# Kernel optimization log

Measured on AMD Instinct MI355X. Metric: run time of the kernel, lower is better.

## Reference

```python
import jax, jax.numpy as jnp
import numpy as np

N_NODES, N_EDGES, NNZ = 10000, 4000, 30000
IN_CH, HEADS, OUT_CH = 128, 2, 64


def _scale2_pattern(node, edge, num_nodes, num_edges):
    """Sparsity pattern of H @ (H^T H) where H is the node x edge incidence.
    Mirrors torch.sparse.mm + coalesce + (values > 0) mask (pattern only,
    since all values are positive sums of ones)."""
    # unique incidence pattern (coalesce)
    uk = np.unique(node.astype(np.int64) * num_edges + edge.astype(np.int64))
    n_u, e_u = uk // num_edges, uk % num_edges
    # --- stage 1: pattern of H^T H = edge pairs sharing a node ---
    order = np.argsort(n_u, kind="stable")
    ns, es = n_u[order], e_u[order]
    _, starts, cnts = np.unique(ns, return_index=True, return_counts=True)
    cpe = np.repeat(cnts, cnts)          # group size per sorted entry
    gpe = np.repeat(starts, cnts)        # group start per sorted entry
    tot = int(cpe.sum())
    within = np.arange(tot) - np.repeat(np.cumsum(cpe) - cpe, cpe)
    pe = np.repeat(es, cpe)
    pep = es[np.repeat(gpe, cpe) + within]
    pk = np.unique(pe * num_edges + pep)
    pe, pep = pk // num_edges, pk % num_edges
    # --- stage 2: pattern of H @ (H^T H) ---
    po = np.argsort(pe, kind="stable")
    pe_s, pep_s = pe[po], pep[po]
    cnt_e = np.bincount(pe_s, minlength=num_edges)
    ptr = np.concatenate([np.zeros(1, np.int64), np.cumsum(cnt_e)])
    c2 = cnt_e[e_u]
    tot2 = int(c2.sum())
    within2 = np.arange(tot2) - np.repeat(np.cumsum(c2) - c2, c2)
    v2 = np.repeat(n_u, c2)
    ep2 = pep_s[ptr[e_u].repeat(c2) + within2]
    k2 = np.unique(v2 * num_edges + ep2)
    return k2 // num_edges, k2 % num_edges


def setup_inputs() -> dict:
    rng = np.random.default_rng(0)
    node1 = rng.integers(0, N_NODES, NNZ).astype(np.int64)
    edge1 = rng.integers(0, N_EDGES, NNZ).astype(np.int64)
    node2, edge2 = _scale2_pattern(node1, edge1, N_NODES, N_EDGES)

    key = jax.random.key(0)
    k = jax.random.split(key, 4)
    HO = HEADS * OUT_CH
    xav1 = (2.0 / (IN_CH + HO)) ** 0.5
    xavo = (2.0 / (HO + OUT_CH)) ** 0.5
    return {
        "x": jax.random.normal(k[0], (N_NODES, IN_CH), jnp.float32),
        "hyperedge_index1": jnp.asarray(np.stack([node1, edge1]), jnp.int32),
        "hyperedge_index2": jnp.asarray(np.stack([node2, edge2]), jnp.int32),
        "W1": jax.random.normal(k[1], (HO, IN_CH), jnp.float32) * xav1,
        "b1": jnp.zeros((HO,), jnp.float32),
        "W2": jax.random.normal(k[2], (HO, IN_CH), jnp.float32) * xav1,
        "b2": jnp.zeros((HO,), jnp.float32),
        "Wout": jax.random.normal(k[3], (OUT_CH, HO), jnp.float32) * xavo,
        "bout": jnp.zeros((OUT_CH,), jnp.float32),
        "num_edges": N_EDGES,
    }


def _hconv(x, W, b, node_idx, edge_idx, num_edges):
    num_nodes = x.shape[0]
    xt = x @ W.T + b                                  # [N, H*O]
    g = xt[node_idx]                                  # [nnz, H*O] gather
    esum = jax.ops.segment_sum(g, edge_idx, num_segments=num_edges)
    cnt = jax.ops.segment_sum(jnp.ones(edge_idx.shape, xt.dtype), edge_idx,
                              num_segments=num_edges)
    emean = esum / jnp.maximum(cnt, 1.0)[:, None]     # scatter_mean (0 if empty)
    return jax.ops.segment_sum(emean[edge_idx], node_idx,
                               num_segments=num_nodes)  # scatter_add


def reference(x, hyperedge_index1, hyperedge_index2, W1, b1, W2, b2, Wout, bout,
              num_edges):
    o1 = _hconv(x, W1, b1, hyperedge_index1[0], hyperedge_index1[1], num_edges)
    o2 = _hconv(x, W2, b2, hyperedge_index2[0], hyperedge_index2[1], num_edges)
    o = 0.5 * (o1 + o2)                               # mean over 2 scales
    return o @ Wout.T + bout                          # output_proj
```

## Files before the change

kernel.cpp:

```cpp
#include <hip/hip_runtime.h>
#include <hip/hip_bf16.h>

#define N_NODES 10000
#define N_EDGES 4000
#define IN_CH   128
#define HOC     128
#define OUT_CH  64
#define CHUNK   16384

#define G_GEMM  625
#define G_NPTR  40

__device__ __forceinline__ float bf2f(unsigned short u) {
    union { unsigned int i; float f; } v;
    v.i = ((unsigned int)u) << 16;
    return v.f;
}
__device__ __forceinline__ unsigned short f2bfu(float f) {
    union { __hip_bfloat16 h; unsigned short u; } v;
    v.h = __float2bfloat16(f);
    return v.u;
}

__device__ __forceinline__ void load8(const void* base, size_t eoff, int isf32,
                                      float o[8]) {
    if (isf32) {
        const float4* q = (const float4*)((const float*)base + eoff);
        float4 a = q[0], b = q[1];
        o[0]=a.x; o[1]=a.y; o[2]=a.z; o[3]=a.w;
        o[4]=b.x; o[5]=b.y; o[6]=b.z; o[7]=b.w;
    } else {
        uint4 v = *(const uint4*)((const unsigned short*)base + eoff);
        const unsigned short* pv = (const unsigned short*)&v;
#pragma unroll
        for (int q = 0; q < 8; q++) o[q] = bf2f(pv[q]);
    }
}

__device__ __forceinline__ float loadS(const void* base, int i, int isf32) {
    return isf32 ? ((const float*)base)[i] : bf2f(((const unsigned short*)base)[i]);
}

__device__ __forceinline__ int probe_isf32(const unsigned int* __restrict__ x) {
    const int lane = threadIdx.x & 63;
    unsigned int w0 = x[lane * 2], w1 = x[lane * 2 + 1];
    int h = 0, z = 0;
    {
        unsigned int lo = w0 & 0xFFFFu;
        if (lo == 0u) z++; else if (((lo >> 7) & 0xFF) >= 0x90u) h++;
        lo = w1 & 0xFFFFu;
        if (lo == 0u) z++; else if (((lo >> 7) & 0xFF) >= 0x90u) h++;
    }
    unsigned long long bh = __ballot(h > 0);
    unsigned long long bz = __ballot(z == 2);
    return (__popcll(bh) > 8 || __popcll(bz) > 50) ? 1 : 0;
}

__device__ __forceinline__ void add4(float acc[4], uint2 u) {
    acc[0] += bf2f((unsigned short)(u.x & 0xFFFFu));
    acc[1] += bf2f((unsigned short)(u.x >> 16));
    acc[2] += bf2f((unsigned short)(u.y & 0xFFFFu));
    acc[3] += bf2f((unsigned short)(u.y >> 16));
}

__global__ __launch_bounds__(256) void weff_zero(
    const void* __restrict__ Wout,
    const void* __restrict__ W1, const void* __restrict__ b1,
    const void* __restrict__ W2, const void* __restrict__ b2,
    float* __restrict__ weff1, float* __restrict__ beff1,
    float* __restrict__ weff2, float* __restrict__ beff2,
    int* __restrict__ cntz, int* __restrict__ fillz,
    const unsigned int* __restrict__ xprobe)
{
    const int b = blockIdx.x;
    if (b == 16) {
        for (int t = threadIdx.x; t < 18000; t += 256) cntz[t] = 0;
        for (int t = threadIdx.x; t < 14000; t += 256) fillz[t] = 0;
        return;
    }
    const int isf32 = probe_isf32(xprobe);
    if (b == 17) {
        const int t = threadIdx.x;
        if (t < 128) {
            const int s = t >> 6, o = t & 63;
            const void* bs = s ? b2 : b1;
            float a = 0.f;
            for (int h = 0; h < 128; h++)
                a += loadS(Wout, o * 128 + h, isf32) * loadS(bs, h, isf32);
            (s ? beff2 : beff1)[o] = 0.5f * a;
        }
        return;
    }
    const int s = b >> 3;
    const void* Ws = s ? W2 : W1;
    float* outW = s ? weff2 : weff1;
    const int o  = (b & 7) * 8 + (threadIdx.x >> 5);
    const int i0 = (threadIdx.x & 31) * 4;
    float acc[4] = {0.f, 0.f, 0.f, 0.f};
    for (int h = 0; h < 128; h++) {
        float wo = loadS(Wout, o * 128 + h, isf32);
        acc[0] += wo * loadS(Ws, h * 128 + i0 + 0, isf32);
        acc[1] += wo * loadS(Ws, h * 128 + i0 + 1, isf32);
        acc[2] += wo * loadS(Ws, h * 128 + i0 + 2, isf32);
        acc[3] += wo * loadS(Ws, h * 128 + i0 + 3, isf32);
    }
    *(float4*)(outW + o * 128 + i0) =
        make_float4(0.5f * acc[0], 0.5f * acc[1], 0.5f * acc[2], 0.5f * acc[3]);
}

__global__ __launch_bounds__(256) void prep(
    const void* __restrict__ x,
    const float* __restrict__ weff1, const float* __restrict__ beff1,
    const float* __restrict__ weff2, const float* __restrict__ beff2,
    unsigned short* __restrict__ xtP1b, unsigned short* __restrict__ xtP2b,
    const int* __restrict__ idx1, int nnz1,
    const int* __restrict__ idx2, int nnz2,
    int* __restrict__ nptr,
    int* __restrict__ bh, int* __restrict__ cnt2,
    int* __restrict__ cnt1e, int* __restrict__ cnt1n, int nblk)
{
    __shared__ __align__(16) char smem[40000];
    int b = blockIdx.x;

    if (b < nblk) {
        int* h = (int*)smem;
        for (int t = threadIdx.x; t < N_EDGES; t += 256) h[t] = 0;
        __syncthreads();
        const int lo = b * CHUNK;
        const int hi = min(nnz2, lo + CHUNK);
        for (int i = lo + threadIdx.x; i < hi; i += 256)
            atomicAdd(&h[idx2[nnz2 + i]], 1);
        __syncthreads();
        int* dst = bh + (size_t)b * N_EDGES;
        for (int t = threadIdx.x; t < N_EDGES; t += 256) {
            int v = h[t];
            dst[t] = v;
            if (v) atomicAdd(&cnt2[t], v);
        }
        return;
    }
    b -= nblk;

    if (b < 8) {
        const int isEdge = b < 4;
        const int bid = isEdge ? b : (b - 4);
        const int nb = isEdge ? N_EDGES : N_NODES;
        const int* src = isEdge ? (idx1 + nnz1) : idx1;
        int* dst = isEdge ? cnt1e : cnt1n;
        int* h = (int*)smem;
        for (int t = threadIdx.x; t < nb; t += 256) h[t] = 0;
        __syncthreads();
        for (int i = bid * 256 + threadIdx.x; i < nnz1; i += 4 * 256)
            atomicAdd(&h[src[i]], 1);
        __syncthreads();
        for (int t = threadIdx.x; t < nb; t += 256) {
            int v = h[t];
            if (v) atomicAdd(&dst[t], v);
        }
        return;
    }
    b -= 8;

    if (b < G_GEMM) {
        const int isf32 = probe_isf32((const unsigned int*)x);
        float (*xs)[IN_CH] = (float (*)[IN_CH])smem;
        const int n0 = b * 16;
        {
            float v[8];
            load8(x, (size_t)n0 * IN_CH + (size_t)threadIdx.x * 8, isf32, v);
            float* dst = &xs[0][0] + threadIdx.x * 8;
#pragma unroll
            for (int q = 0; q < 8; q++) dst[q] = v[q];
        }
        __syncthreads();

        const int g   = threadIdx.x >> 7;
        const int sel = (threadIdx.x >> 6) & 1;
        const int j   = threadIdx.x & 63;
        const float* WE = sel ? weff2 : weff1;
        const float* BE = sel ? beff2 : beff1;
        unsigned short* xtP = sel ? xtP2b : xtP1b;

        float acc[8];
#pragma unroll
        for (int m = 0; m < 8; m++) acc[m] = 0.f;

        const float4* Wr = (const float4*)(WE + (size_t)j * 128);
        for (int kk = 0; kk < 16; kk++) {
            float4 a = Wr[kk * 2], c = Wr[kk * 2 + 1];
            float w[8] = {a.x, a.y, a.z, a.w, c.x, c.y, c.z, c.w};
#pragma unroll
            for (int m = 0; m < 8; m++) {
                const float* xr = &xs[g * 8 + m][kk * 8];
                acc[m] += xr[0]*w[0] + xr[1]*w[1] + xr[2]*w[2] + xr[3]*w[3]
                        + xr[4]*w[4] + xr[5]*w[5] + xr[6]*w[6] + xr[7]*w[7];
            }
        }
        const float bias = BE[j];
#pragma unroll
        for (int m = 0; m < 8; m++)
            xtP[(size_t)(n0 + g * 8 + m) * 64 + j] = f2bfu(acc[m] + bias);
        return;
    }
    b -= G_GEMM;

    {
        int n = b * 256 + threadIdx.x;
        if (n > N_NODES) return;
        int lo = 0, hi = nnz2;
        while (lo < hi) { int mid = (lo + hi) >> 1; if (idx2[mid] < n) lo = mid + 1; else hi = mid; }
        nptr[n] = lo;
    }
}

__global__ __launch_bounds__(256) void scans3(
    const int* __restrict__ cnt2, int* __restrict__ ptr2,
    const int* __restrict__ cnt1e, int* __restrict__ ptr1e,
    const int* __restrict__ cnt1n, int* __restrict__ ptr1n)
{
    const int* cnt; int* ptr; int nb;
    if (blockIdx.x == 0)      { cnt = cnt2;  ptr = ptr2;  nb = N_EDGES; }
    else if (blockIdx.x == 1) { cnt = cnt1e; ptr = ptr1e; nb = N_EDGES; }
    else                      { cnt = cnt1n; ptr = ptr1n; nb = N_NODES; }
    __shared__ int part[256];
    const int t = threadIdx.x;
    const int K = (nb + 255) >> 8;
    const int base = t * K;
    int s = 0;
    for (int q = 0; q < K; q++) {
        int i = base + q;
        s += (i < nb) ? cnt[i] : 0;
    }
    part[t] = s;
    __syncthreads();
    for (int d = 1; d < 256; d <<= 1) {
        int v = (t >= d) ? part[t - d] : 0;
        __syncthreads();
        part[t] += v;
        __syncthreads();
    }
    int run = part[t] - s;
    for (int q = 0; q < K; q++) {
        int i = base + q;
        if (i < nb) { ptr[i] = run; run += cnt[i]; }
    }
    if (t == 255) ptr[nb] = part[255];
}

__global__ __launch_bounds__(256) void sb_fb(
    const int* __restrict__ ptr2, int* __restrict__ bh, int nblk,
    const int* __restrict__ idx1, int nnz1,
    const int* __restrict__ ptr1e, int* __restrict__ fill1e,
    unsigned short* __restrict__ nodelist1,
    const int* __restrict__ ptr1n, int* __restrict__ fill1n,
    unsigned short* __restrict__ edgelist1)
{
    int b = blockIdx.x;
    if (b < 16) {
        int e = b * 256 + threadIdx.x;
        if (e >= N_EDGES) return;
        int run = ptr2[e];
        int k = 0;
        for (; k + 8 <= nblk; k += 8) {
            int v[8];
#pragma unroll
            for (int q = 0; q < 8; q++)
                v[q] = bh[(size_t)(k + q) * N_EDGES + e];
#pragma unroll
            for (int q = 0; q < 8; q++) {
                bh[(size_t)(k + q) * N_EDGES + e] = run;
                run += v[q];
            }
        }
        for (; k < nblk; k++) {
            int i = k * N_EDGES + e;
            int t = bh[i];
            bh[i] = run;
            run += t;
        }
        return;
    }
    b -= 16;
    int i = b * 256 + threadIdx.x;
    if (i >= nnz1) return;
    int n = idx1[i];
    int e = idx1[nnz1 + i];
    int se = atomicAdd(&fill1e[e], 1);
    nodelist1[ptr1e[e] + se] = (unsigned short)n;
    int sn = atomicAdd(&fill1n[n], 1);
    edgelist1[ptr1n[n] + sn] = (unsigned short)e;
}

__global__ __launch_bounds__(1024) void place_entries(
    const int* __restrict__ idx, int nnz, const int* __restrict__ bh,
    unsigned short* __restrict__ nodelist)
{
    __shared__ int lh[N_EDGES];
    for (int t = threadIdx.x; t < N_EDGES; t += 1024) lh[t] = 0;
    __syncthreads();
    const int b = blockIdx.x;
    const int lo = b * CHUNK;
    const int hi = min(nnz, lo + CHUNK);
    const int* bhb = bh + (size_t)b * N_EDGES;
    for (int i = lo + threadIdx.x; i < hi; i += 1024) {
        int n = idx[i];
        int e = idx[nnz + i];
        int s = atomicAdd(&lh[e], 1);
        nodelist[bhb[e] + s] = (unsigned short)n;
    }
}

__global__ __launch_bounds__(256) void edge_gather(
    const unsigned short* __restrict__ nodelist2, const int* __restrict__ ptr2,
    const unsigned int* __restrict__ xtP2u, unsigned int* __restrict__ emean2b,
    const unsigned short* __restrict__ nodelist1, const int* __restrict__ ptr1e,
    const unsigned int* __restrict__ xtP1u, unsigned int* __restrict__ emean1b)
{
    int b = blockIdx.x;
    if (b < 1000) {
        const int lane = threadIdx.x & 63;
        const int sub  = lane >> 4;
        const int ch4  = lane & 15;
        const int e = b * 4 + (threadIdx.x >> 6);
        const int lo = ptr2[e], hi = ptr2[e + 1];
        const uint2* src2 = (const uint2*)xtP2u;
        float acc[4] = {0.f, 0.f, 0.f, 0.f};
        int i = lo;
        for (; i + 32 <= hi; i += 32) {
            int n[8]; uint2 u[8];
#pragma unroll
            for (int q = 0; q < 8; q++) n[q] = nodelist2[i + 4 * q + sub];
#pragma unroll
            for (int q = 0; q < 8; q++) u[q] = src2[(size_t)n[q] * 16 + ch4];
#pragma unroll
            for (int q = 0; q < 8; q++) add4(acc, u[q]);
        }
        for (; i < hi; i += 4) {
            if (i + sub < hi) {
                int n0 = nodelist2[i + sub];
                add4(acc, src2[(size_t)n0 * 16 + ch4]);
            }
        }
#pragma unroll
        for (int q = 0; q < 4; q++) {
            acc[q] += __shfl_xor(acc[q], 16);
            acc[q] += __shfl_xor(acc[q], 32);
        }
        if (sub == 0) {
            const float inv = 1.f / fmaxf((float)(hi - lo), 1.f);
            uint2 o;
            o.x = ((unsigned int)f2bfu(acc[1] * inv) << 16) | f2bfu(acc[0] * inv);
            o.y = ((unsigned int)f2bfu(acc[3] * inv) << 16) | f2bfu(acc[2] * inv);
            ((uint2*)emean2b)[(size_t)e * 16 + ch4] = o;
        }
        return;
    }
    b -= 1000;
    {
        const int lane = threadIdx.x & 31;
        const int e = b * 8 + (threadIdx.x >> 5);
        const int lo = ptr1e[e], hi = ptr1e[e + 1];
        float accx = 0.f, accy = 0.f;
        for (int base = lo; base < hi; base += 32) {
            const int m = min(32, hi - base);
            int vl = (base + lane < hi) ? (int)nodelist1[base + lane] : 0;
            int t = 0;
            for (; t + 7 < m; t += 8) {
                int nn[8]; unsigned int uu[8];
#pragma unroll
                for (int q = 0; q < 8; q++) nn[q] = __shfl(vl, t + q, 32);
#pragma unroll
                for (int q = 0; q < 8; q++) uu[q] = xtP1u[nn[q] * 32 + lane];
#pragma unroll
                for (int q = 0; q < 8; q++) {
                    accx += bf2f((unsigned short)(uu[q] & 0xFFFFu));
                    accy += bf2f((unsigned short)(uu[q] >> 16));
                }
            }
            for (; t < m; t++) {
                int n = __shfl(vl, t, 32);
                unsigned int u = xtP1u[n * 32 + lane];
                accx += bf2f((unsigned short)(u & 0xFFFFu));
                accy += bf2f((unsigned short)(u >> 16));
            }
        }
        const float inv = 1.f / fmaxf((float)(hi - lo), 1.f);
        emean1b[e * 32 + lane] =
            ((unsigned int)f2bfu(accy * inv) << 16) | f2bfu(accx * inv);
    }
}

__global__ __launch_bounds__(256) void node_final(
    const int* __restrict__ vals2, const int* __restrict__ nptr,
    const unsigned int* __restrict__ emean2b,
    const unsigned short* __restrict__ edgelist1, const int* __restrict__ ptr1n,
    const unsigned int* __restrict__ emean1b,
    const void* __restrict__ bout, void* __restrict__ out,
    const unsigned int* __restrict__ xprobe)
{
    const int isf32 = probe_isf32(xprobe);
    const int lane = threadIdx.x & 63;
    const int sub  = lane >> 4;
    const int ch4  = lane & 15;
    const int n = blockIdx.x * 4 + (threadIdx.x >> 6);
    float acc[4] = {0.f, 0.f, 0.f, 0.f};

    {
        const int lo = nptr[n], hi = nptr[n + 1];
        const uint2* src = (const uint2*)emean2b;
        int i = lo;
        for (; i + 32 <= hi; i += 32) {
            int e[8]; uint2 u[8];
#pragma unroll
            for (int q = 0; q < 8; q++) e[q] = vals2[i + 4 * q + sub];
#pragma unroll
            for (int q = 0; q < 8; q++) u[q] = src[(size_t)e[q] * 16 + ch4];
#pragma unroll
            for (int q = 0; q < 8; q++) add4(acc, u[q]);
        }
        for (; i < hi; i += 4) {
            if (i + sub < hi)
                add4(acc, src[(size_t)vals2[i + sub] * 16 + ch4]);
        }
    }
    {
        const int lo = ptr1n[n], hi = ptr1n[n + 1];
        const uint2* src = (const uint2*)emean1b;
        int i = lo;
        for (; i + 32 <= hi; i += 32) {
            int e[8]; uint2 u[8];
#pragma unroll
            for (int q = 0; q < 8; q++) e[q] = edgelist1[i + 4 * q + sub];
#pragma unroll
            for (int q = 0; q < 8; q++) u[q] = src[(size_t)e[q] * 16 + ch4];
#pragma unroll
            for (int q = 0; q < 8; q++) add4(acc, u[q]);
        }
        for (; i < hi; i += 4) {
            if (i + sub < hi)
                add4(acc, src[(size_t)edgelist1[i + sub] * 16 + ch4]);
        }
    }
#pragma unroll
    for (int q = 0; q < 4; q++) {
        acc[q] += __shfl_xor(acc[q], 16);
        acc[q] += __shfl_xor(acc[q], 32);
    }
    if (sub == 0) {
        float r[4];
#pragma unroll
        for (int q = 0; q < 4; q++)
            r[q] = acc[q] + loadS(bout, ch4 * 4 + q, isf32);
        if (isf32) {
            ((float4*)out)[(size_t)n * 16 + ch4] =
                make_float4(r[0], r[1], r[2], r[3]);
        } else {
            uint2 o;
            o.x = ((unsigned int)f2bfu(r[1]) << 16) | f2bfu(r[0]);
            o.y = ((unsigned int)f2bfu(r[3]) << 16) | f2bfu(r[2]);
            ((uint2*)out)[(size_t)n * 16 + ch4] = o;
        }
    }
}

extern "C" void kernel_launch(void* const* d_in, const int* in_sizes, int n_in,
                              void* d_out, int out_size, void* d_ws, size_t ws_size,
                              hipStream_t stream)
{
    const void* x  = d_in[0];
    const int* idx1 = (const int*)d_in[1];
    const int* idx2 = (const int*)d_in[2];
    const void* W1 = d_in[3];
    const void* b1 = d_in[4];
    const void* W2 = d_in[5];
    const void* b2 = d_in[6];
    const void* Wo = d_in[7];
    const void* bo = d_in[8];

    const int nnz1 = in_sizes[1] / 2;
    const int nnz2 = in_sizes[2] / 2;
    const int nblk = (nnz2 + CHUNK - 1) / CHUNK;

    float* ws = (float*)d_ws;
    unsigned short* xtP1b = (unsigned short*)ws;
    unsigned int*   xtP1u = (unsigned int*)xtP1b;
    unsigned short* xtP2b = (unsigned short*)(ws + 320000);
    unsigned int*   xtP2u = (unsigned int*)xtP2b;
    int*   fill1e = (int*)(ws + 1280000);
    int*   fill1n = (int*)(ws + 1284000);
    int* cnt2  = (int*)(ws + 1550000);
    int* cnt1e = (int*)(ws + 1554000);
    int* cnt1n = (int*)(ws + 1558000);
    int* ptr2  = (int*)(ws + 1568000);
    int* ptr1e = (int*)(ws + 1572004);
    int* ptr1n = (int*)(ws + 1576008);
    int* nptr  = (int*)(ws + 1586012);
    float* weff1 = ws + 1596016;
    float* weff2 = ws + 1604208;
    float* beff1 = ws + 1612400;
    float* beff2 = ws + 1612464;
    unsigned int* emean2b = (unsigned int*)(ws + 1612528);
    unsigned int* emean1b = (unsigned int*)(ws + 1740528);
    unsigned short* nodelist2 = (unsigned short*)(ws + 1868528);
    const size_t nl2u = ((size_t)nnz2 + 1) / 2;
    unsigned short* nodelist1 = (unsigned short*)(ws + 1868528 + nl2u);
    const size_t nl1u = ((size_t)nnz1 + 1) / 2;
    unsigned short* edgelist1 = (unsigned short*)(ws + 1868528 + nl2u + nl1u);
    const size_t bh_off = (1868528 + nl2u + 2 * nl1u + 7) & ~(size_t)7;
    int* bh = (int*)(ws + bh_off);

    weff_zero<<<18, 256, 0, stream>>>(Wo, W1, b1, W2, b2,
                                      weff1, beff1, weff2, beff2,
                                      cnt2, fill1e, (const unsigned int*)x);

    prep<<<nblk + 8 + G_GEMM + G_NPTR, 256, 0, stream>>>(
        x, weff1, beff1, weff2, beff2, xtP1b, xtP2b,
        idx1, nnz1, idx2, nnz2,
        nptr, bh, cnt2, cnt1e, cnt1n, nblk);

    scans3<<<3, 256, 0, stream>>>(cnt2, ptr2, cnt1e, ptr1e, cnt1n, ptr1n);

    sb_fb<<<16 + (nnz1 + 255) / 256, 256, 0, stream>>>(
        ptr2, bh, nblk, idx1, nnz1, ptr1e, fill1e, nodelist1,
        ptr1n, fill1n, edgelist1);

    place_entries<<<nblk, 1024, 0, stream>>>(idx2, nnz2, bh, nodelist2);

    edge_gather<<<1000 + N_EDGES / 8, 256, 0, stream>>>(
        nodelist2, ptr2, xtP2u, emean2b,
        nodelist1, ptr1e, xtP1u, emean1b);

    node_final<<<N_NODES / 4, 256, 0, stream>>>(
        idx2 + nnz2, nptr, emean2b, edgelist1, ptr1n, emean1b,
        bo, d_out, (const unsigned int*)x);
}
```

Measured before the change: 225.9 us.

## Tile Wout·W weight folding through shared memory with register-blocked outputs

The weight-folding kernel that computes Wout·W1 and Wout·W2 now stages 64-row slices of W in shared memory. Each thread keeps a 64-element row slice of Wout in registers and accumulates 16 outputs, replacing the earlier per-element strided global loads. The grid drops from 18 blocks to 6, and the bias-folding block stages the biases in shared memory and uses vectorised loads. Each block now does more work with less parallelism and higher register pressure, in exchange for far fewer redundant global reads.

Result: faster. 198.5 us (-12.1%).

```diff
diff --git a/kernel.cpp b/kernel.cpp
--- a/kernel.cpp
+++ b/kernel.cpp
@@ -73,39 +73,77 @@
     const unsigned int* __restrict__ xprobe)
 {
     const int b = blockIdx.x;
-    if (b == 16) {
+    if (b == 4) {
         for (int t = threadIdx.x; t < 18000; t += 256) cntz[t] = 0;
         for (int t = threadIdx.x; t < 14000; t += 256) fillz[t] = 0;
         return;
     }
+    __shared__ float wsh[64][IN_CH];
     const int isf32 = probe_isf32(xprobe);
-    if (b == 17) {
+
+    if (b == 5) {
+        float* bsh = &wsh[0][0];
         const int t = threadIdx.x;
+        {
+            const int s = t >> 7, h = t & 127;
+            bsh[t] = loadS(s ? b2 : b1, h, isf32);
+        }
+        __syncthreads();
         if (t < 128) {
             const int s = t >> 6, o = t & 63;
-            const void* bs = s ? b2 : b1;
             float a = 0.f;
-            for (int h = 0; h < 128; h++)
-                a += loadS(Wout, o * 128 + h, isf32) * loadS(bs, h, isf32);
+#pragma unroll 4
+            for (int r = 0; r < 16; r++) {
+                float v[8];
+                load8(Wout, (size_t)o * 128 + r * 8, isf32, v);
+#pragma unroll
+                for (int q = 0; q < 8; q++) a += v[q] * bsh[s * 128 + r * 8 + q];
+            }
             (s ? beff2 : beff1)[o] = 0.5f * a;
         }
         return;
     }
-    const int s = b >> 3;
+
+    const int s  = b >> 1;
+    const int oh = b & 1;
     const void* Ws = s ? W2 : W1;
     float* outW = s ? weff2 : weff1;
-    const int o  = (b & 7) * 8 + (threadIdx.x >> 5);
-    const int i0 = (threadIdx.x & 31) * 4;
-    float acc[4] = {0.f, 0.f, 0.f, 0.f};
-    for (int h = 0; h < 128; h++) {
-        float wo = loadS(Wout, o * 128 + h, isf32);
-        acc[0] += wo * loadS(Ws, h * 128 + i0 + 0, isf32);
-        acc[1] += wo * loadS(Ws, h * 128 + i0 + 1, isf32);
-        acc[2] += wo * loadS(Ws, h * 128 + i0 + 2, isf32);
-        acc[3] += wo * loadS(Ws, h * 128 + i0 + 3, isf32);
-    }
-    *(float4*)(outW + o * 128 + i0) =
-        make_float4(0.5f * acc[0], 0.5f * acc[1], 0.5f * acc[2], 0.5f * acc[3]);
+    const int o  = oh * 32 + (threadIdx.x >> 3);
+    const int i0 = (threadIdx.x & 7) * 16;
+    float acc[16];
+#pragma unroll
+    for (int k = 0; k < 16; k++) acc[k] = 0.f;
+
+    for (int pass = 0; pass < 2; pass++) {
+        if (pass) __syncthreads();
+        for (int r = 0; r < 4; r++) {
+            int idx = r * 2048 + threadIdx.x * 8;
+            float v[8];
+            load8(Ws, (size_t)pass * 8192 + idx, isf32, v);
+            float* d = &wsh[0][0] + idx;
+#pragma unroll
+            for (int q = 0; q < 8; q++) d[q] = v[q];
+        }
+        float wrow[64];
+#pragma unroll
+        for (int r = 0; r < 8; r++) {
+            float v[8];
+            load8(Wout, (size_t)o * 128 + pass * 64 + r * 8, isf32, v);
+#pragma unroll
+            for (int q = 0; q < 8; q++) wrow[r * 8 + q] = v[q];
+        }
+        __syncthreads();
+#pragma unroll 4
+        for (int h = 0; h < 64; h++) {
+            const float wo = wrow[h];
+            const float* wr = &wsh[h][i0];
+#pragma unroll
+            for (int k = 0; k < 16; k++) acc[k] += wo * wr[k];
+        }
+    }
+#pragma unroll
+    for (int k = 0; k < 16; k++)
+        outW[o * 128 + i0 + k] = 0.5f * acc[k];
 }
 
 __global__ __launch_bounds__(256) void prep(
@@ -509,9 +547,9 @@
     const size_t bh_off = (1868528 + nl2u + 2 * nl1u + 7) & ~(size_t)7;
     int* bh = (int*)(ws + bh_off);
 
-    weff_zero<<<18, 256, 0, stream>>>(Wo, W1, b1, W2, b2,
-                                      weff1, beff1, weff2, beff2,
-                                      cnt2, fill1e, (const unsigned int*)x);
+    weff_zero<<<6, 256, 0, stream>>>(Wo, W1, b1, W2, b2,
+                                     weff1, beff1, weff2, beff2,
+                                     cnt2, fill1e, (const unsigned int*)x);
 
     prep<<<nblk + 8 + G_GEMM + G_NPTR, 256, 0, stream>>>(
         x, weff1, beff1, weff2, beff2, xtP1b, xtP2b,
```
